# Kernel tuning notes

Measured on AMD Instinct MI355X. Metric: run time of the kernel, lower is better.

Reference implementation:

```python
import jax, jax.numpy as jnp
import numpy as np

N_EMBD = 128
N_HEADS = 8
HEAD_SIZE = N_EMBD // N_HEADS  # 16
EPS = 1e-5


def _layernorm(x, g, b):
    m = jnp.mean(x, axis=-1, keepdims=True)
    v = jnp.mean(jnp.square(x - m), axis=-1, keepdims=True)
    return (x - m) * jax.lax.rsqrt(v + EPS) * g + b


def setup_inputs() -> dict:
    key = jax.random.key(0)
    ks = jax.random.split(key, 12)
    B, T, D, H, HS = 16, 1024, N_EMBD, N_HEADS, HEAD_SIZE
    s = 1.0 / np.sqrt(D)
    inp = {
        "x": jax.random.normal(ks[0], (B, T, D), jnp.float32),
        # per-head QKV projections (stacked over heads; matches ModuleList of Linear(D, HS))
        "Wq": jax.random.uniform(ks[1], (H, D, HS), jnp.float32, -s, s),
        "bq": jnp.zeros((H, HS), jnp.float32),
        "Wk": jax.random.uniform(ks[2], (H, D, HS), jnp.float32, -s, s),
        "bk": jnp.zeros((H, HS), jnp.float32),
        "Wv": jax.random.uniform(ks[3], (H, D, HS), jnp.float32, -s, s),
        "bv": jnp.zeros((H, HS), jnp.float32),
        "Wp": jax.random.uniform(ks[4], (H * HS, D), jnp.float32, -s, s),
        "bp": jnp.zeros((D,), jnp.float32),
        "W1": jax.random.uniform(ks[5], (D, 4 * D), jnp.float32, -s, s),
        "b1": jnp.zeros((4 * D,), jnp.float32),
        "W2": jax.random.uniform(ks[6], (4 * D, D), jnp.float32, -1.0 / np.sqrt(4 * D), 1.0 / np.sqrt(4 * D)),
        "b2": jnp.zeros((D,), jnp.float32),
        "g1": jnp.ones((D,), jnp.float32),
        "be1": jnp.zeros((D,), jnp.float32),
        "g2": jnp.ones((D,), jnp.float32),
        "be2": jnp.zeros((D,), jnp.float32),
    }
    return inp


def reference(x, Wq, bq, Wk, bk, Wv, bv, Wp, bp, W1, b1, W2, b2, g1, be1, g2, be2):
    B, T, D = x.shape
    # batched per-head projections: [B,T,D] x [H,D,HS] -> [B,H,T,HS]
    q = jnp.einsum("btd,hds->bhts", x, Wq) + bq[None, :, None, :]
    k = jnp.einsum("btd,hds->bhts", x, Wk) + bk[None, :, None, :]
    v = jnp.einsum("btd,hds->bhts", x, Wv) + bv[None, :, None, :]
    scores = jnp.einsum("bhts,bhus->bhtu", q, k) / np.sqrt(HEAD_SIZE).astype(np.float32)
    tril = jnp.tril(jnp.ones((T, T), x.dtype))
    # faithful to source: multiplicative + additive mask (not -inf where)
    scores = scores * tril - 1e12 * (1.0 - tril)
    attn = jax.nn.softmax(scores, axis=-1)
    out = jnp.einsum("bhtu,bhus->bhts", attn, v)  # [B,H,T,HS]
    # concat heads in head order -> [B,T,H*HS]
    out = out.transpose(0, 2, 1, 3).reshape(B, T, -1)
    attn_out = out @ Wp + bp
    x = _layernorm(attn_out + x, g1, be1)
    h = jax.nn.gelu(x @ W1 + b1, approximate=False) @ W2 + b2
    x = _layernorm(h + x, g2, be2)
    return x
```

## Files before the change

kernel.cpp:

```cpp
#include <hip/hip_runtime.h>
#include <hip/hip_bf16.h>
#include <math.h>

constexpr int NB  = 16;
constexpr int NT  = 1024;
constexpr int ND  = 128;
constexpr int NH  = 8;
constexpr int NHS = 16;
constexpr int NDH = 512;
constexpr long NBT = (long)NB * NT;

typedef __attribute__((ext_vector_type(8))) short short8;
typedef __attribute__((ext_vector_type(4))) float f32x4;
typedef __attribute__((ext_vector_type(16))) float f32x16;
typedef __attribute__((ext_vector_type(4))) unsigned short us4;

__device__ __forceinline__ unsigned short f2bf(float f) {
    __hip_bfloat16 h = __float2bfloat16(f);
    return *(unsigned short*)&h;
}

__device__ __forceinline__ short8 cvt8(const float* p) {
    const float4 f0 = *(const float4*)p;
    const float4 f1 = *(const float4*)(p + 4);
    union { short8 s; __hip_bfloat162 h[4]; } u;
    u.h[0] = __float22bfloat162_rn(make_float2(f0.x, f0.y));
    u.h[1] = __float22bfloat162_rn(make_float2(f0.z, f0.w));
    u.h[2] = __float22bfloat162_rn(make_float2(f1.x, f1.y));
    u.h[3] = __float22bfloat162_rn(make_float2(f1.z, f1.w));
    return u.s;
}

__device__ __forceinline__ float fast_gelu(float y) {
    const float t = y * y;
    const float u = __builtin_fmaf(y * 0.044715f, t, y);
    const float e = __builtin_amdgcn_exp2f(u * -2.302118131f);
    return y * __builtin_amdgcn_rcpf(1.0f + e);
}

__global__ __launch_bounds__(256) void k_prep(
    const float* __restrict__ Wq, const float* __restrict__ Wk,
    const float* __restrict__ Wv, __hip_bfloat16* __restrict__ Wqkvt)
{
    const int blk = blockIdx.x, tid = threadIdx.x;
    const int i0 = blk * 1024 + tid * 4;
    const int n = i0 >> 7, d0 = i0 & 127;
    const int sec = n >> 7, m = n & 127;
    const float* W = (sec == 0) ? Wq : (sec == 1) ? Wk : Wv;
    const float* src = W + (m >> 4) * 2048 + (m & 15);
    us4 v;
    #pragma unroll
    for (int j = 0; j < 4; ++j) v[j] = f2bf(src[(d0 + j) * 16]);
    *(us4*)((unsigned short*)Wqkvt + i0) = v;
}

__global__ __launch_bounds__(256) void k_qkv(
    const float* __restrict__ x, const __hip_bfloat16* __restrict__ Wqkvt,
    const float* __restrict__ bq, const float* __restrict__ bk,
    const float* __restrict__ bv,
    const float* __restrict__ Wp, const float* __restrict__ W1,
    const float* __restrict__ W2,
    __hip_bfloat16* __restrict__ Wpt, __hip_bfloat16* __restrict__ W1t,
    __hip_bfloat16* __restrict__ W2t,
    __hip_bfloat16* __restrict__ qo, __hip_bfloat16* __restrict__ ko,
    __hip_bfloat16* __restrict__ vo)
{
    __shared__ __align__(16) unsigned short st[32 * 392];
    const int tid = threadIdx.x;

    if (blockIdx.x >= 512) {
        const int blk = blockIdx.x - 512 + 48;
        us4 v;
        if (blk < 64) {
            const int i0 = (blk - 48) * 1024 + tid * 4;
            const int n = i0 >> 7, d0 = i0 & 127;
            #pragma unroll
            for (int j = 0; j < 4; ++j) v[j] = f2bf(Wp[(d0 + j) * 128 + n]);
            *(us4*)((unsigned short*)Wpt + i0) = v;
        } else if (blk < 128) {
            const int i0 = (blk - 64) * 1024 + tid * 4;
            const int n = i0 >> 7, d0 = i0 & 127;
            #pragma unroll
            for (int j = 0; j < 4; ++j) v[j] = f2bf(W1[(d0 + j) * 512 + n]);
            *(us4*)((unsigned short*)W1t + i0) = v;
        } else {
            const int i0 = (blk - 128) * 1024 + tid * 4;
            const int n = i0 >> 9, k0 = i0 & 511;
            #pragma unroll
            for (int j = 0; j < 4; ++j) v[j] = f2bf(W2[(k0 + j) * 128 + n]);
            *(us4*)((unsigned short*)W2t + i0) = v;
        }
        return;
    }

    const int w    = tid >> 6;
    const int lane = tid & 63;
    const int sL   = lane & 15;
    const int quad = lane >> 4;
    const int tok0 = blockIdx.x * 32;

    const unsigned short* W = (const unsigned short*)Wqkvt;

    short8 bx[2][4];
    #pragma unroll
    for (int tt = 0; tt < 2; ++tt)
        #pragma unroll
        for (int ks = 0; ks < 4; ++ks)
            bx[tt][ks] = cvt8(x + (size_t)(tok0 + tt * 16 + sL) * 128 + ks * 32 + quad * 8);

    f32x4 acc[6][2];
    #pragma unroll
    for (int ci = 0; ci < 6; ++ci)
        #pragma unroll
        for (int tt = 0; tt < 2; ++tt)
            acc[ci][tt] = (f32x4){0.f, 0.f, 0.f, 0.f};

    #pragma unroll
    for (int ks = 0; ks < 4; ++ks) {
        short8 aW[6];
        #pragma unroll
        for (int ci = 0; ci < 6; ++ci) {
            const int ct = w * 6 + ci;
            aW[ci] = *(const short8*)(W + (size_t)(ct * 16 + sL) * 128 + ks * 32 + quad * 8);
        }
        #pragma unroll
        for (int ci = 0; ci < 6; ++ci)
            #pragma unroll
            for (int tt = 0; tt < 2; ++tt)
                acc[ci][tt] = __builtin_amdgcn_mfma_f32_16x16x32_bf16(aW[ci], bx[tt][ks], acc[ci][tt], 0, 0, 0);
    }

    const float qscale = 0.3606737602f;
    #pragma unroll
    for (int ci = 0; ci < 6; ++ci) {
        const int ct = w * 6 + ci;
        const int kind = ct >> 3;
        const int ncc = (ct & 7) * 16 + quad * 4;
        const float4 bb = *(const float4*)(((kind == 0) ? bq : (kind == 1) ? bk : bv) + ncc);
        #pragma unroll
        for (int tt = 0; tt < 2; ++tt) {
            us4 v;
            #pragma unroll
            for (int r = 0; r < 4; ++r) {
                float val = acc[ci][tt][r] + ((const float*)&bb)[r];
                if (kind == 0) val *= qscale;
                v[r] = f2bf(val);
            }
            *(us4*)(st + (tt * 16 + sL) * 392 + ct * 16 + quad * 4) = v;
        }
    }
    __syncthreads();

    const int b = tok0 >> 10, tt0 = tok0 & 1023;
    {
        const int h = tid >> 5, tok = tid & 31;
        const unsigned short* sq = st + tok * 392 + h * 16;
        const unsigned short* sk = st + tok * 392 + 128 + h * 16;
        unsigned short* dq = (unsigned short*)qo + ((size_t)(b * 8 + h) * 1024 + tt0 + tok) * 16;
        unsigned short* dk = (unsigned short*)ko + ((size_t)(b * 8 + h) * 1024 + tt0 + tok) * 16;
        *(short8*)dq       = *(const short8*)sq;
        *(short8*)(dq + 8) = *(const short8*)(sq + 8);
        *(short8*)dk       = *(const short8*)sk;
        *(short8*)(dk + 8) = *(const short8*)(sk + 8);
    }
    if (tid < 128) {
        const int h = tid >> 4, s = tid & 15;
        unsigned short tmp[32];
        #pragma unroll
        for (int tok = 0; tok < 32; ++tok)
            tmp[tok] = st[tok * 392 + 256 + h * 16 + s];
        unsigned short* dv = (unsigned short*)vo + ((size_t)(b * 8 + h) * 16 + s) * 1024 + tt0;
        #pragma unroll
        for (int j = 0; j < 4; ++j)
            *(short8*)(dv + j * 8) = *(const short8*)(tmp + j * 8);
    }
}

__global__ __launch_bounds__(256) void k_attn(
    const __hip_bfloat16* __restrict__ qb, const __hip_bfloat16* __restrict__ kb,
    const __hip_bfloat16* __restrict__ vtb, __hip_bfloat16* __restrict__ att)
{
    __shared__ __align__(16) float stg[4][32 * 16];
    const int bh   = blockIdx.x & 127;
    const int sub  = blockIdx.x >> 7;
    const int wave = threadIdx.x >> 6;
    const int lane = threadIdx.x & 63;
    const int col  = lane & 31;
    const int hi   = lane >> 5;
    const int b = bh >> 3, h = bh & 7;
    const int tile = sub * 4 + wave;
    const int t0 = tile * 32;

    const unsigned short* qp = (const unsigned short*)qb  + (size_t)bh * NT * NHS;
    const unsigned short* kp = (const unsigned short*)kb  + (size_t)bh * NT * NHS;
    const unsigned short* vp = (const unsigned short*)vtb + (size_t)bh * NHS * NT;

    const short8 bQ = *(const short8*)(qp + (size_t)(t0 + col) * NHS + hi * 8);
    const unsigned short* vrow = vp + (size_t)(col & 15) * NT + hi * 8;

    f32x16 o;
    #pragma unroll
    for (int r = 0; r < 16; ++r) o[r] = 0.f;
    f32x16 zc;
    #pragma unroll
    for (int r = 0; r < 16; ++r) zc[r] = 0.f;
    float lp0 = 0.f, lp1 = 0.f, lp2 = 0.f, lp3 = 0.f;

    for (int c = 0; c <= tile; ++c) {
        const int u0 = c * 32;
        const short8 aK  = *(const short8*)(kp + (size_t)(u0 + col) * NHS + hi * 8);
        const short8 bV0 = *(const short8*)(vrow + u0);
        const short8 bV1 = *(const short8*)(vrow + u0 + 16);

        const f32x16 sT = __builtin_amdgcn_mfma_f32_32x32x16_bf16(aK, bQ, zc, 0, 0, 0);

        float p[16];
        if (c < tile) {
            #pragma unroll
            for (int r = 0; r < 16; ++r) p[r] = __builtin_amdgcn_exp2f(sT[r]);
        } else {
            const int kh = 4 * hi;
            #pragma unroll
            for (int r = 0; r < 16; ++r) {
                const int kc = (r & 3) + 8 * (r >> 2) + kh;
                const float e = __builtin_amdgcn_exp2f(sT[r]);
                p[r] = (kc <= col) ? e : 0.f;
            }
        }
        #pragma unroll
        for (int r = 0; r < 16; r += 4) {
            lp0 += p[r]; lp1 += p[r + 1]; lp2 += p[r + 2]; lp3 += p[r + 3];
        }

        int d[8];
        #pragma unroll
        for (int i = 0; i < 8; ++i) {
            __hip_bfloat162 hh = __float22bfloat162_rn(make_float2(p[2 * i], p[2 * i + 1]));
            d[i] = *(int*)&hh;
        }
        auto s0 = __builtin_amdgcn_permlane32_swap(d[0], d[2], false, false);
        auto s1 = __builtin_amdgcn_permlane32_swap(d[1], d[3], false, false);
        auto s2 = __builtin_amdgcn_permlane32_swap(d[4], d[6], false, false);
        auto s3 = __builtin_amdgcn_permlane32_swap(d[5], d[7], false, false);
        union { int i[4]; short8 v; } A0, A1;
        A0.i[0] = s0[0]; A0.i[1] = s1[0]; A0.i[2] = s0[1]; A0.i[3] = s1[1];
        A1.i[0] = s2[0]; A1.i[1] = s3[0]; A1.i[2] = s2[1]; A1.i[3] = s3[1];

        o = __builtin_amdgcn_mfma_f32_32x32x16_bf16(A0.v, bV0, o, 0, 0, 0);
        o = __builtin_amdgcn_mfma_f32_32x32x16_bf16(A1.v, bV1, o, 0, 0, 0);
    }

    float lp = (lp0 + lp1) + (lp2 + lp3);
    lp += __shfl_xor(lp, 32);
    const float inv = 1.0f / lp;

    float* sp = stg[wave];
    if (col < 16) {
        #pragma unroll
        for (int r = 0; r < 16; ++r) {
            const int qr = (r & 3) + 8 * (r >> 2) + 4 * hi;
            sp[qr * 16 + col] = o[r];
        }
    }
    __syncthreads();
    const float invq = __shfl(inv, lane >> 1);
    const float* rp = sp + (lane >> 1) * 16 + (lane & 1) * 8;
    const float4 va = *(const float4*)rp;
    const float4 vb = *(const float4*)(rp + 4);
    union { short8 v; unsigned short u[8]; } res;
    res.u[0] = f2bf(va.x * invq); res.u[1] = f2bf(va.y * invq);
    res.u[2] = f2bf(va.z * invq); res.u[3] = f2bf(va.w * invq);
    res.u[4] = f2bf(vb.x * invq); res.u[5] = f2bf(vb.y * invq);
    res.u[6] = f2bf(vb.z * invq); res.u[7] = f2bf(vb.w * invq);
    unsigned short* dst = (unsigned short*)att +
        ((size_t)b * NT + t0 + (lane >> 1)) * ND + h * NHS + (lane & 1) * 8;
    *(short8*)dst = res.v;
}

__global__ __launch_bounds__(256) void k_tail(
    const __hip_bfloat16* __restrict__ attb, const __hip_bfloat16* __restrict__ Wpt,
    const __hip_bfloat16* __restrict__ W1t, const __hip_bfloat16* __restrict__ W2t,
    const float* __restrict__ x, const float* __restrict__ bp,
    const float* __restrict__ g1, const float* __restrict__ be1,
    const float* __restrict__ b1, const float* __restrict__ b2,
    const float* __restrict__ g2, const float* __restrict__ be2,
    float* __restrict__ out)
{
    __shared__ float ys[32][132];
    __shared__ __align__(16) unsigned short l1b[32 * 136];
    __shared__ __align__(16) unsigned short midb[32 * 528];
    const int w    = threadIdx.x >> 6;
    const int lane = threadIdx.x & 63;
    const int sL   = lane & 15;
    const int quad = lane >> 4;
    const int tok0 = blockIdx.x * 32;

    {
        const unsigned short* A = (const unsigned short*)attb;
        const unsigned short* W = (const unsigned short*)Wpt;
        short8 bfr[2][4];
        #pragma unroll
        for (int tt = 0; tt < 2; ++tt)
            #pragma unroll
            for (int ks = 0; ks < 4; ++ks)
                bfr[tt][ks] = *(const short8*)(A + (size_t)(tok0 + tt * 16 + sL) * 128 + ks * 32 + quad * 8);

        f32x4 acc[2][2];
        #pragma unroll
        for (int ci = 0; ci < 2; ++ci)
            #pragma unroll
            for (int tt = 0; tt < 2; ++tt)
                acc[ci][tt] = (f32x4){0.f, 0.f, 0.f, 0.f};

        #pragma unroll
        for (int ks = 0; ks < 4; ++ks) {
            short8 aW[2];
            #pragma unroll
            for (int ci = 0; ci < 2; ++ci)
                aW[ci] = *(const short8*)(W + (size_t)((w * 2 + ci) * 16 + sL) * 128 + ks * 32 + quad * 8);
            #pragma unroll
            for (int ci = 0; ci < 2; ++ci)
                #pragma unroll
                for (int tt = 0; tt < 2; ++tt)
                    acc[ci][tt] = __builtin_amdgcn_mfma_f32_16x16x32_bf16(aW[ci], bfr[tt][ks], acc[ci][tt], 0, 0, 0);
        }
        #pragma unroll
        for (int ci = 0; ci < 2; ++ci) {
            const int n0 = (w * 2 + ci) * 16 + quad * 4;
            const float4 bb = *(const float4*)(bp + n0);
            #pragma unroll
            for (int tt = 0; tt < 2; ++tt) {
                float4 v;
                v.x = acc[ci][tt][0] + bb.x; v.y = acc[ci][tt][1] + bb.y;
                v.z = acc[ci][tt][2] + bb.z; v.w = acc[ci][tt][3] + bb.w;
                *(float4*)(&ys[tt * 16 + sL][n0]) = v;
            }
        }
    }
    __syncthreads();

    const int tok = threadIdx.x >> 3;
    const int l8  = threadIdx.x & 7;
    const int c0  = l8 * 16;
    {
        float vals[16];
        float s = 0.f, s2 = 0.f;
        #pragma unroll
        for (int ch = 0; ch < 4; ++ch) {
            const float4 ly = *(const float4*)&ys[tok][c0 + ch * 4];
            const float4 gx = *(const float4*)(x + (size_t)(tok0 + tok) * 128 + c0 + ch * 4);
            vals[ch*4+0] = ly.x + gx.x; vals[ch*4+1] = ly.y + gx.y;
            vals[ch*4+2] = ly.z + gx.z; vals[ch*4+3] = ly.w + gx.w;
            #pragma unroll
            for (int j = 0; j < 4; ++j) { s += vals[ch*4+j]; s2 += vals[ch*4+j] * vals[ch*4+j]; }
        }
        #pragma unroll
        for (int off = 1; off <= 4; off <<= 1) {
            s  += __shfl_xor(s, off, 8);
            s2 += __shfl_xor(s2, off, 8);
        }
        const float mean = s * (1.0f / 128.0f);
        const float var  = s2 * (1.0f / 128.0f) - mean * mean;
        const float rstd = rsqrtf(var + 1e-5f);
        #pragma unroll
        for (int ch = 0; ch < 4; ++ch) {
            const float4 gg = *(const float4*)(g1 + c0 + ch * 4);
            const float4 bb = *(const float4*)(be1 + c0 + ch * 4);
            float ln0 = (vals[ch*4+0] - mean) * rstd * gg.x + bb.x;
            float ln1v = (vals[ch*4+1] - mean) * rstd * gg.y + bb.y;
            float ln2v = (vals[ch*4+2] - mean) * rstd * gg.z + bb.z;
            float ln3 = (vals[ch*4+3] - mean) * rstd * gg.w + bb.w;
            ys[tok][c0 + ch*4 + 0] = ln0;
            ys[tok][c0 + ch*4 + 1] = ln1v;
            ys[tok][c0 + ch*4 + 2] = ln2v;
            ys[tok][c0 + ch*4 + 3] = ln3;
            us4 lb;
            lb[0] = f2bf(ln0); lb[1] = f2bf(ln1v); lb[2] = f2bf(ln2v); lb[3] = f2bf(ln3);
            *(us4*)(l1b + tok * 136 + c0 + ch * 4) = lb;
        }
    }
    __syncthreads();

    {
        const unsigned short* W = (const unsigned short*)W1t;
        short8 bl[2][4];
        #pragma unroll
        for (int tt = 0; tt < 2; ++tt)
            #pragma unroll
            for (int ks = 0; ks < 4; ++ks)
                bl[tt][ks] = *(const short8*)(l1b + (tt * 16 + sL) * 136 + ks * 32 + quad * 8);

        f32x4 acc[8][2];
        #pragma unroll
        for (int ci = 0; ci < 8; ++ci)
            #pragma unroll
            for (int tt = 0; tt < 2; ++tt)
                acc[ci][tt] = (f32x4){0.f, 0.f, 0.f, 0.f};

        #pragma unroll
        for (int ks = 0; ks < 4; ++ks) {
            short8 aW[8];
            #pragma unroll
            for (int ci = 0; ci < 8; ++ci)
                aW[ci] = *(const short8*)(W + (size_t)((w * 8 + ci) * 16 + sL) * 128 + ks * 32 + quad * 8);
            #pragma unroll
            for (int ci = 0; ci < 8; ++ci)
                #pragma unroll
                for (int tt = 0; tt < 2; ++tt)
                    acc[ci][tt] = __builtin_amdgcn_mfma_f32_16x16x32_bf16(aW[ci], bl[tt][ks], acc[ci][tt], 0, 0, 0);
        }
        #pragma unroll
        for (int ci = 0; ci < 8; ++ci) {
            const int n0 = (w * 8 + ci) * 16 + quad * 4;
            const float4 bb = *(const float4*)(b1 + n0);
            #pragma unroll
            for (int tt = 0; tt < 2; ++tt) {
                us4 v;
                v[0] = f2bf(fast_gelu(acc[ci][tt][0] + bb.x));
                v[1] = f2bf(fast_gelu(acc[ci][tt][1] + bb.y));
                v[2] = f2bf(fast_gelu(acc[ci][tt][2] + bb.z));
                v[3] = f2bf(fast_gelu(acc[ci][tt][3] + bb.w));
                *(us4*)(midb + (tt * 16 + sL) * 528 + n0) = v;
            }
        }
    }
    __syncthreads();

    f32x4 acc2[2][2];
    #pragma unroll
    for (int ci = 0; ci < 2; ++ci)
        #pragma unroll
        for (int tt = 0; tt < 2; ++tt)
            acc2[ci][tt] = (f32x4){0.f, 0.f, 0.f, 0.f};
    {
        const unsigned short* W = (const unsigned short*)W2t;
        #pragma unroll
        for (int ks = 0; ks < 16; ++ks) {
            short8 bm0 = *(const short8*)(midb + (size_t)sL * 528 + ks * 32 + quad * 8);
            short8 bm1 = *(const short8*)(midb + (size_t)(16 + sL) * 528 + ks * 32 + quad * 8);
            short8 aW0 = *(const short8*)(W + (size_t)((w * 2) * 16 + sL) * 512 + ks * 32 + quad * 8);
            short8 aW1 = *(const short8*)(W + (size_t)((w * 2 + 1) * 16 + sL) * 512 + ks * 32 + quad * 8);
            acc2[0][0] = __builtin_amdgcn_mfma_f32_16x16x32_bf16(aW0, bm0, acc2[0][0], 0, 0, 0);
            acc2[0][1] = __builtin_amdgcn_mfma_f32_16x16x32_bf16(aW0, bm1, acc2[0][1], 0, 0, 0);
            acc2[1][0] = __builtin_amdgcn_mfma_f32_16x16x32_bf16(aW1, bm0, acc2[1][0], 0, 0, 0);
            acc2[1][1] = __builtin_amdgcn_mfma_f32_16x16x32_bf16(aW1, bm1, acc2[1][1], 0, 0, 0);
        }
    }
    __syncthreads();
    float* ys2 = (float*)midb;
    #pragma unroll
    for (int ci = 0; ci < 2; ++ci) {
        const int n0 = (w * 2 + ci) * 16 + quad * 4;
        const float4 bb = *(const float4*)(b2 + n0);
        #pragma unroll
        for (int tt = 0; tt < 2; ++tt) {
            float4 v;
            v.x = acc2[ci][tt][0] + bb.x; v.y = acc2[ci][tt][1] + bb.y;
            v.z = acc2[ci][tt][2] + bb.z; v.w = acc2[ci][tt][3] + bb.w;
            *(float4*)(ys2 + (tt * 16 + sL) * 132 + n0) = v;
        }
    }
    __syncthreads();

    {
        float vals[16];
        float s = 0.f, s2 = 0.f;
        #pragma unroll
        for (int ch = 0; ch < 4; ++ch) {
            const float4 ly = *(const float4*)(ys2 + tok * 132 + c0 + ch * 4);
            const float4 gx = *(const float4*)&ys[tok][c0 + ch * 4];
            vals[ch*4+0] = ly.x + gx.x; vals[ch*4+1] = ly.y + gx.y;
            vals[ch*4+2] = ly.z + gx.z; vals[ch*4+3] = ly.w + gx.w;
            #pragma unroll
            for (int j = 0; j < 4; ++j) { s += vals[ch*4+j]; s2 += vals[ch*4+j] * vals[ch*4+j]; }
        }
        #pragma unroll
        for (int off = 1; off <= 4; off <<= 1) {
            s  += __shfl_xor(s, off, 8);
            s2 += __shfl_xor(s2, off, 8);
        }
        const float mean = s * (1.0f / 128.0f);
        const float var  = s2 * (1.0f / 128.0f) - mean * mean;
        const float rstd = rsqrtf(var + 1e-5f);
        #pragma unroll
        for (int ch = 0; ch < 4; ++ch) {
            const float4 gg = *(const float4*)(g2 + c0 + ch * 4);
            const float4 bb = *(const float4*)(be2 + c0 + ch * 4);
            float4 ln;
            ln.x = (vals[ch*4+0] - mean) * rstd * gg.x + bb.x;
            ln.y = (vals[ch*4+1] - mean) * rstd * gg.y + bb.y;
            ln.z = (vals[ch*4+2] - mean) * rstd * gg.z + bb.z;
            ln.w = (vals[ch*4+3] - mean) * rstd * gg.w + bb.w;
            *(float4*)(out + (size_t)(tok0 + tok) * 128 + c0 + ch * 4) = ln;
        }
    }
}

extern "C" void kernel_launch(void* const* d_in, const int* in_sizes, int n_in,
                              void* d_out, int out_size, void* d_ws, size_t ws_size,
                              hipStream_t stream)
{
    (void)in_sizes; (void)n_in; (void)out_size; (void)ws_size;
    const float* x   = (const float*)d_in[0];
    const float* Wq  = (const float*)d_in[1];
    const float* bq  = (const float*)d_in[2];
    const float* Wk  = (const float*)d_in[3];
    const float* bk  = (const float*)d_in[4];
    const float* Wv  = (const float*)d_in[5];
    const float* bv  = (const float*)d_in[6];
    const float* Wp  = (const float*)d_in[7];
    const float* bp  = (const float*)d_in[8];
    const float* W1  = (const float*)d_in[9];
    const float* b1  = (const float*)d_in[10];
    const float* W2  = (const float*)d_in[11];
    const float* b2  = (const float*)d_in[12];
    const float* g1  = (const float*)d_in[13];
    const float* be1 = (const float*)d_in[14];
    const float* g2  = (const float*)d_in[15];
    const float* be2 = (const float*)d_in[16];
    float* out = (float*)d_out;

    char* wsb = (char*)d_ws;
    __hip_bfloat16* qb   = (__hip_bfloat16*)wsb;
    __hip_bfloat16* kb   = (__hip_bfloat16*)(wsb + (4u  << 20));
    __hip_bfloat16* vtb  = (__hip_bfloat16*)(wsb + (8u  << 20));
    __hip_bfloat16* attb = (__hip_bfloat16*)(wsb + (12u << 20));
    __hip_bfloat16* Wqkvt= (__hip_bfloat16*)(wsb + (16u << 20));
    __hip_bfloat16* Wpt  = (__hip_bfloat16*)(wsb + (16u << 20) + (96u  << 10));
    __hip_bfloat16* W1t  = (__hip_bfloat16*)(wsb + (16u << 20) + (128u << 10));
    __hip_bfloat16* W2t  = (__hip_bfloat16*)(wsb + (16u << 20) + (256u << 10));

    k_prep<<<48,   256, 0, stream>>>(Wq, Wk, Wv, Wqkvt);
    k_qkv <<<656,  256, 0, stream>>>(x, Wqkvt, bq, bk, bv, Wp, W1, W2,
                                     Wpt, W1t, W2t, qb, kb, vtb);
    k_attn<<<1024, 256, 0, stream>>>(qb, kb, vtb, attb);
    k_tail<<<512,  256, 0, stream>>>(attb, Wpt, W1t, W2t, x, bp, g1, be1,
                                     b1, b2, g2, be2, out);
}
```

Measured before the change: 160.0 us.

## Fuse QKV weight conversion into projection kernel and rebalance attention tile mapping

After: 154.4 us. -3.5%, faster.

```diff
diff --git a/kernel.cpp b/kernel.cpp
--- a/kernel.cpp
+++ b/kernel.cpp
@@ -31,6 +31,14 @@
     return u.s;
 }
 
+__device__ __forceinline__ short8 cvt8s(const float* p) {
+    union { short8 s; __hip_bfloat162 h[4]; } u;
+    #pragma unroll
+    for (int jj = 0; jj < 4; ++jj)
+        u.h[jj] = __float22bfloat162_rn(make_float2(p[(2 * jj) * 16], p[(2 * jj + 1) * 16]));
+    return u.s;
+}
+
 __device__ __forceinline__ float fast_gelu(float y) {
     const float t = y * y;
     const float u = __builtin_fmaf(y * 0.044715f, t, y);
@@ -38,24 +46,10 @@
     return y * __builtin_amdgcn_rcpf(1.0f + e);
 }
 
-__global__ __launch_bounds__(256) void k_prep(
+__global__ __launch_bounds__(256) void k_qkv(
+    const float* __restrict__ x,
     const float* __restrict__ Wq, const float* __restrict__ Wk,
-    const float* __restrict__ Wv, __hip_bfloat16* __restrict__ Wqkvt)
-{
-    const int blk = blockIdx.x, tid = threadIdx.x;
-    const int i0 = blk * 1024 + tid * 4;
-    const int n = i0 >> 7, d0 = i0 & 127;
-    const int sec = n >> 7, m = n & 127;
-    const float* W = (sec == 0) ? Wq : (sec == 1) ? Wk : Wv;
-    const float* src = W + (m >> 4) * 2048 + (m & 15);
-    us4 v;
-    #pragma unroll
-    for (int j = 0; j < 4; ++j) v[j] = f2bf(src[(d0 + j) * 16]);
-    *(us4*)((unsigned short*)Wqkvt + i0) = v;
-}
-
-__global__ __launch_bounds__(256) void k_qkv(
-    const float* __restrict__ x, const __hip_bfloat16* __restrict__ Wqkvt,
+    const float* __restrict__ Wv,
     const float* __restrict__ bq, const float* __restrict__ bk,
     const float* __restrict__ bv,
     const float* __restrict__ Wp, const float* __restrict__ W1,
@@ -99,8 +93,6 @@
     const int quad = lane >> 4;
     const int tok0 = blockIdx.x * 32;
 
-    const unsigned short* W = (const unsigned short*)Wqkvt;
-
     short8 bx[2][4];
     #pragma unroll
     for (int tt = 0; tt < 2; ++tt)
@@ -121,7 +113,9 @@
         #pragma unroll
         for (int ci = 0; ci < 6; ++ci) {
             const int ct = w * 6 + ci;
-            aW[ci] = *(const short8*)(W + (size_t)(ct * 16 + sL) * 128 + ks * 32 + quad * 8);
+            const int kind = ct >> 3;
+            const float* Wsec = (kind == 0) ? Wq : (kind == 1) ? Wk : Wv;
+            aW[ci] = cvt8s(Wsec + (ct & 7) * 2048 + (ks * 32 + quad * 8) * 16 + sL);
         }
         #pragma unroll
         for (int ci = 0; ci < 6; ++ci)
@@ -188,7 +182,7 @@
     const int col  = lane & 31;
     const int hi   = lane >> 5;
     const int b = bh >> 3, h = bh & 7;
-    const int tile = sub * 4 + wave;
+    const int tile = wave * 8 + sub;
     const int t0 = tile * 32;
 
     const unsigned short* qp = (const unsigned short*)qb  + (size_t)bh * NT * NHS;
@@ -525,13 +519,11 @@
     __hip_bfloat16* kb   = (__hip_bfloat16*)(wsb + (4u  << 20));
     __hip_bfloat16* vtb  = (__hip_bfloat16*)(wsb + (8u  << 20));
     __hip_bfloat16* attb = (__hip_bfloat16*)(wsb + (12u << 20));
-    __hip_bfloat16* Wqkvt= (__hip_bfloat16*)(wsb + (16u << 20));
     __hip_bfloat16* Wpt  = (__hip_bfloat16*)(wsb + (16u << 20) + (96u  << 10));
     __hip_bfloat16* W1t  = (__hip_bfloat16*)(wsb + (16u << 20) + (128u << 10));
     __hip_bfloat16* W2t  = (__hip_bfloat16*)(wsb + (16u << 20) + (256u << 10));
 
-    k_prep<<<48,   256, 0, stream>>>(Wq, Wk, Wv, Wqkvt);
-    k_qkv <<<656,  256, 0, stream>>>(x, Wqkvt, bq, bk, bv, Wp, W1, W2,
+    k_qkv <<<656,  256, 0, stream>>>(x, Wq, Wk, Wv, bq, bk, bv, Wp, W1, W2,
                                      Wpt, W1t, W2t, qb, kb, vtb);
     k_attn<<<1024, 256, 0, stream>>>(qb, kb, vtb, attb);
     k_tail<<<512,  256, 0, stream>>>(attb, Wpt, W1t, W2t, x, bp, g1, be1,
```
